# Kernel optimization log

Hardware: AMD Instinct MI355X
Metric: run time of the kernel (lower is better)

Reference implementation:

```python
import jax, jax.numpy as jnp
import numpy as np

_EPS = 1e-5
_NORM_EPS = 1e-6


def setup_inputs() -> dict:
    key = jax.random.key(0)
    k1, k2 = jax.random.split(key)
    B, S, D_IN, D_OUT = 4, 8192, 2048, 2048
    x = jax.random.normal(k1, (B, S, D_IN), dtype=jnp.float32)
    gamma = jnp.ones((D_IN,), dtype=jnp.float32)  # RMSNorm scale
    # kaiming_uniform-like init: bound = sqrt(6/((1+5)*fan_in)) = 1/sqrt(fan_in)
    bound = 1.0 / np.sqrt(D_IN)
    W = jax.random.uniform(k2, (D_OUT, D_IN), dtype=jnp.float32, minval=-bound, maxval=bound)
    return {"x": x, "gamma": gamma, "W": W}


def reference(x, gamma, W):
    # RMSNorm (pre-norm baked into BitLinear)
    rms = jax.lax.rsqrt(jnp.mean(x * x, axis=-1, keepdims=True) + _NORM_EPS)
    xn = x * rms * gamma

    # Per-token absmax int8 activation fake-quant with STE
    a_scale = 127.0 / (jnp.max(jnp.abs(xn), axis=-1, keepdims=True) + _EPS)
    x_q = jnp.clip(jnp.round(xn * a_scale), -128.0, 127.0) / a_scale
    x_ste = xn + jax.lax.stop_gradient(x_q - xn)

    # Per-tensor ternary weight fake-quant (absmean scale) with STE
    w_scale = 1.0 / (jnp.mean(jnp.abs(W)) + _EPS)
    w_q = jnp.clip(jnp.round(W * w_scale), -1.0, 1.0) / w_scale
    w_ste = W + jax.lax.stop_gradient(w_q - W)

    # Linear: [B,S,Din] x [Dout,Din]^T -> [B,S,Dout]
    return jnp.einsum('bsd,od->bso', x_ste, w_ste)
```

## Files before the change

kernel.cpp:

```cpp
#include <hip/hip_runtime.h>
#include <stdint.h>

#define K_DIM 2048
#define N_DIM 2048
#define M_TOK 32768

typedef float v4f __attribute__((ext_vector_type(4)));
typedef int   v4i __attribute__((ext_vector_type(4)));

#define WS_PART   0
#define WS_STAT   8192
#define WS_TSCALE 8448
#define WS_WT     262144
#define WS_QX     4456448

__device__ __forceinline__ void gload_lds16(const void* g, void* l) {
    __builtin_amdgcn_global_load_lds(
        (const __attribute__((address_space(1))) unsigned int*)g,
        (__attribute__((address_space(3))) unsigned int*)l,
        16, 0, 0);
}

__device__ __forceinline__ unsigned int pack4(int a, int b, int c, int d) {
    return (unsigned int)(a & 255) | ((unsigned int)(b & 255) << 8) |
           ((unsigned int)(c & 255) << 16) | ((unsigned int)(d & 255) << 24);
}

__global__ __launch_bounds__(256) void wabs_partial(const float* __restrict__ W,
                                                    double* __restrict__ part) {
    const int t = threadIdx.x, b = blockIdx.x;
    const float* p = W + (size_t)b * 4096;
    double s = 0.0;
#pragma unroll
    for (int i = 0; i < 4; ++i) {
        float4 v = *(const float4*)(p + i * 1024 + t * 4);
        s += (double)fabsf(v.x) + (double)fabsf(v.y) +
             (double)fabsf(v.z) + (double)fabsf(v.w);
    }
    int lane = t & 63, wv = t >> 6;
#pragma unroll
    for (int off = 32; off > 0; off >>= 1) s += __shfl_down(s, off, 64);
    __shared__ double red[4];
    if (lane == 0) red[wv] = s;
    __syncthreads();
    if (t == 0) part[b] = red[0] + red[1] + red[2] + red[3];
}

__global__ __launch_bounds__(256) void wfinal(const double* __restrict__ part,
                                              float* __restrict__ wstat) {
    const int t = threadIdx.x;
    double s = part[t] + part[t + 256] + part[t + 512] + part[t + 768];
    int lane = t & 63, wv = t >> 6;
#pragma unroll
    for (int off = 32; off > 0; off >>= 1) s += __shfl_down(s, off, 64);
    __shared__ double red[4];
    if (lane == 0) red[wv] = s;
    __syncthreads();
    if (t == 0) {
        double mean = (red[0] + red[1] + red[2] + red[3]) * (1.0 / 4194304.0);
        float winv = (float)mean + 1e-5f;
        wstat[0] = winv;
        wstat[1] = 1.0f / winv;
    }
}

__global__ __launch_bounds__(256) void wquant(const float* __restrict__ W,
                                              const float* __restrict__ wstat,
                                              int8_t* __restrict__ wt) {
    const float wsc = wstat[1];
    size_t i = ((size_t)blockIdx.x * 256 + threadIdx.x) * 4;
    float4 v = *(const float4*)(W + i);
    int q0 = (int)rintf(fminf(fmaxf(v.x * wsc, -1.0f), 1.0f));
    int q1 = (int)rintf(fminf(fmaxf(v.y * wsc, -1.0f), 1.0f));
    int q2 = (int)rintf(fminf(fmaxf(v.z * wsc, -1.0f), 1.0f));
    int q3 = (int)rintf(fminf(fmaxf(v.w * wsc, -1.0f), 1.0f));
    *(unsigned int*)(wt + i) = pack4(q0, q1, q2, q3);
}

__global__ __launch_bounds__(256) void rmsnorm_quant(const float* __restrict__ x,
                                                     const float* __restrict__ gamma,
                                                     const float* __restrict__ wstat,
                                                     int8_t* __restrict__ qx,
                                                     float* __restrict__ tscale) {
    const int row = blockIdx.x;
    const int t = threadIdx.x;
    const float* xr = x + (size_t)row * K_DIM;

    float4 v0 = *(const float4*)(xr + t * 4);
    float4 v1 = *(const float4*)(xr + 1024 + t * 4);
    float4 g0 = *(const float4*)(gamma + t * 4);
    float4 g1 = *(const float4*)(gamma + 1024 + t * 4);

    float ss = v0.x * v0.x + v0.y * v0.y + v0.z * v0.z + v0.w * v0.w +
               v1.x * v1.x + v1.y * v1.y + v1.z * v1.z + v1.w * v1.w;

    __shared__ float red[8];
    {
        int lane = t & 63, wv = t >> 6;
#pragma unroll
        for (int off = 32; off > 0; off >>= 1) ss += __shfl_down(ss, off, 64);
        if (lane == 0) red[wv] = ss;
        __syncthreads();
        ss = red[0] + red[1] + red[2] + red[3];
    }
    const float rms = 1.0f / sqrtf(ss * (1.0f / 2048.0f) + 1e-6f);

    float xn[8];
    xn[0] = v0.x * rms * g0.x;  xn[1] = v0.y * rms * g0.y;
    xn[2] = v0.z * rms * g0.z;  xn[3] = v0.w * rms * g0.w;
    xn[4] = v1.x * rms * g1.x;  xn[5] = v1.y * rms * g1.y;
    xn[6] = v1.z * rms * g1.z;  xn[7] = v1.w * rms * g1.w;

    float am = 0.0f;
#pragma unroll
    for (int j = 0; j < 8; ++j) am = fmaxf(am, fabsf(xn[j]));
    {
        int lane = t & 63, wv = t >> 6;
#pragma unroll
        for (int off = 32; off > 0; off >>= 1) am = fmaxf(am, __shfl_down(am, off, 64));
        if (lane == 0) red[4 + wv] = am;
        __syncthreads();
        am = fmaxf(fmaxf(red[4], red[5]), fmaxf(red[6], red[7]));
    }
    const float amp = am + 1e-5f;
    const float ascale = 127.0f / amp;

    int q[8];
#pragma unroll
    for (int j = 0; j < 8; ++j)
        q[j] = (int)rintf(fminf(fmaxf(xn[j] * ascale, -128.0f), 127.0f));

    int8_t* qr = qx + (size_t)row * K_DIM;
    *(unsigned int*)(qr + t * 4)        = pack4(q[0], q[1], q[2], q[3]);
    *(unsigned int*)(qr + 1024 + t * 4) = pack4(q[4], q[5], q[6], q[7]);

    if (t == 0) tscale[row] = amp * wstat[0] * (1.0f / 127.0f);
}


__device__ __forceinline__ v4i ldsfrag(const int8_t* p, int row, int j0) {
    return *(const v4i*)(p + row * 128 + (((j0) ^ (row & 7)) << 4));
}

template <int Q, bool LOADB>
__device__ __forceinline__ void ph_load(const int8_t* pA, const int8_t* pB,
                                        v4i (&af)[2][2], v4i (&bf)[4][2],
                                        int wm, int wn, int l16, int quad) {
    if constexpr (LOADB) {
#pragma unroll
        for (int nt = 0; nt < 4; ++nt)
#pragma unroll
            for (int ks = 0; ks < 2; ++ks)
                bf[nt][ks] = ldsfrag(pB, wn + nt * 16 + l16, ks * 4 + quad);
    }
#pragma unroll
    for (int mt = 0; mt < 2; ++mt)
#pragma unroll
        for (int ks = 0; ks < 2; ++ks)
            af[mt][ks] = ldsfrag(pA, wm + (2 * Q + mt) * 16 + l16, ks * 4 + quad);
}

template <int Q>
__device__ __forceinline__ void ph_mma(v4i (&acc)[8][4], const v4i (&af)[2][2],
                                       const v4i (&bf)[4][2]) {
#pragma unroll
    for (int mt = 0; mt < 2; ++mt)
#pragma unroll
        for (int nt = 0; nt < 4; ++nt)
#pragma unroll
            for (int ks = 0; ks < 2; ++ks)
                acc[2 * Q + mt][nt] = __builtin_amdgcn_mfma_i32_16x16x64_i8(
                    af[mt][ks], bf[nt][ks], acc[2 * Q + mt][nt], 0, 0, 0);
}

#define VMC(n) asm volatile("s_waitcnt vmcnt(" #n ")" ::: "memory")

__global__ __launch_bounds__(512, 2) void gemm_i8(const int8_t* __restrict__ qx,
                                                  const int8_t* __restrict__ wt,
                                                  const float* __restrict__ tscale,
                                                  float* __restrict__ out) {
    __shared__ int8_t ldsA[2][32768];
    __shared__ int8_t ldsB[2][32768];

    const int t = threadIdx.x;
    const int lane = t & 63;
    const int w = t >> 6;
    const int l16 = lane & 15;
    const int quad = lane >> 4;

    const int bid = blockIdx.x;
    const int swz = (bid & 7) * 128 + (bid >> 3);
    const int bn0 = (swz & 7) * 256;
    const int bm0 = (swz >> 3) * 256;

    const int wm = (w >> 2) * 128;
    const int wn = (w & 3) * 64;

    const int srow = t >> 3;
    const int sjx  = ((t & 7) ^ (srow & 7)) << 4;
    const int wbase = w * 1024;
    const size_t baseA = (size_t)bm0 * K_DIM;
    const size_t baseB = (size_t)bn0 * K_DIM;

#define STAGE_A(buf, h, kt) do {                                                   \
        const int8_t* _s = qx + baseA + (size_t)((h) * 128 + srow) * K_DIM +       \
                           (kt) * 128 + sjx;                                       \
        gload_lds16(_s,              &ldsA[buf][(h) * 16384 + wbase]);             \
        gload_lds16(_s + 64 * K_DIM, &ldsA[buf][(h) * 16384 + 8192 + wbase]);      \
    } while (0)
#define STAGE_B(buf, h, kt) do {                                                   \
        const int8_t* _s = wt + baseB + (size_t)((h) * 128 + srow) * K_DIM +       \
                           (kt) * 128 + sjx;                                       \
        gload_lds16(_s,              &ldsB[buf][(h) * 16384 + wbase]);             \
        gload_lds16(_s + 64 * K_DIM, &ldsB[buf][(h) * 16384 + 8192 + wbase]);      \
    } while (0)

    v4i acc[8][4];
    const v4i izero = {0, 0, 0, 0};
#pragma unroll
    for (int i = 0; i < 8; ++i)
#pragma unroll
        for (int j = 0; j < 4; ++j) acc[i][j] = izero;

    v4i bf[4][2];
    const int8_t* pA0 = ldsA[0];
    const int8_t* pA1 = ldsA[1];
    const int8_t* pB0 = ldsB[0];
    const int8_t* pB1 = ldsB[1];

    STAGE_B(0, 0, 0);
    STAGE_B(0, 1, 0);
    STAGE_A(0, 0, 0);
    STAGE_A(0, 1, 0);
    STAGE_B(1, 0, 1);
    STAGE_B(1, 1, 1);
    VMC(4);
    __builtin_amdgcn_s_barrier();

#define DO_PHASE(Q, LOADB, PA, PB, STAGE_STMT, TAIL_STMT)           \
    {                                                               \
        v4i af[2][2];                                               \
        ph_load<Q, LOADB>(PA, PB, af, bf, wm, wn, l16, quad);       \
        STAGE_STMT;                                                 \
        __builtin_amdgcn_s_barrier();                               \
        asm volatile("s_waitcnt lgkmcnt(0)" ::: "memory");          \
        __builtin_amdgcn_sched_barrier(0);                          \
        __builtin_amdgcn_s_setprio(1);                              \
        ph_mma<Q>(acc, af, bf);                                     \
        __builtin_amdgcn_s_setprio(0);                              \
        TAIL_STMT;                                                  \
        __builtin_amdgcn_s_barrier();                               \
    }

#pragma unroll 1
    for (int i = 0; i < 8; ++i) {
        const int kt1 = 2 * i + 1;
        const int kt2 = 2 * i + 2;
        const int kt3 = 2 * i + 3;
        const bool pf = (i < 7);
        DO_PHASE(0, true,  pA0, pB0, STAGE_A(1, 0, kt1), (void)0);
        DO_PHASE(1, false, pA0, pB0, STAGE_A(1, 1, kt1), (void)0);
        DO_PHASE(2, false, pA0, pB0, if (pf) STAGE_B(0, 0, kt2), (void)0);
        DO_PHASE(3, false, pA0, pB0, if (pf) STAGE_B(0, 1, kt2),
                 if (pf) { VMC(4); } else { VMC(0); });
        DO_PHASE(0, true,  pA1, pB1, if (pf) STAGE_A(0, 0, kt2), (void)0);
        DO_PHASE(1, false, pA1, pB1, if (pf) STAGE_A(0, 1, kt2), (void)0);
        DO_PHASE(2, false, pA1, pB1, if (pf) STAGE_B(1, 0, kt3), (void)0);
        DO_PHASE(3, false, pA1, pB1, if (pf) STAGE_B(1, 1, kt3), VMC(4));
    }

#pragma unroll
    for (int mt = 0; mt < 8; ++mt) {
#pragma unroll
        for (int r = 0; r < 4; ++r) {
            const int row = bm0 + wm + mt * 16 + quad * 4 + r;
            const float s = tscale[row];
            float* op = out + (size_t)row * N_DIM + bn0 + wn + l16;
#pragma unroll
            for (int nt = 0; nt < 4; ++nt)
                op[nt * 16] = (float)acc[mt][nt][r] * s;
        }
    }
#undef DO_PHASE
#undef STAGE_A
#undef STAGE_B
}

extern "C" void kernel_launch(void* const* d_in, const int* in_sizes, int n_in,
                              void* d_out, int out_size, void* d_ws, size_t ws_size,
                              hipStream_t stream) {
    const float* x     = (const float*)d_in[0];
    const float* gamma = (const float*)d_in[1];
    const float* W     = (const float*)d_in[2];
    float* out = (float*)d_out;

    char* ws = (char*)d_ws;
    double* wpart  = (double*)(ws + WS_PART);
    float*  wstat  = (float*)(ws + WS_STAT);
    float*  tscale = (float*)(ws + WS_TSCALE);
    int8_t* wt     = (int8_t*)(ws + WS_WT);
    int8_t* qx     = (int8_t*)(ws + WS_QX);

    wabs_partial<<<1024, 256, 0, stream>>>(W, wpart);
    wfinal<<<1, 256, 0, stream>>>(wpart, wstat);
    wquant<<<4096, 256, 0, stream>>>(W, wstat, wt);
    rmsnorm_quant<<<M_TOK, 256, 0, stream>>>(x, gamma, wstat, qx, tscale);

    gemm_i8<<<dim3(1024), dim3(512), 0, stream>>>(qx, wt, tscale, out);
}
```

Baseline: 595.5 us.

## Software-pipeline LDS fragment loads one phase ahead of MFMA in int8 GEMM

Restructures the main loop so that A fragments for the next phase are loaded from LDS into a second register set while the current phase's MFMAs run, using ping-pong af0/af1 buffers and partial lgkmcnt waits. B fragments are reloaded after the last phase of each K-tile, with one barrier per phase removed. This is meant to hide LDS read latency behind matrix-core work. In exchange it raises register pressure under launch_bounds(512,2) and makes the barrier and waitcnt ordering more delicate.

```diff
diff --git a/kernel.cpp b/kernel.cpp
--- a/kernel.cpp
+++ b/kernel.cpp
@@ -142,27 +142,27 @@
     return *(const v4i*)(p + row * 128 + (((j0) ^ (row & 7)) << 4));
 }
 
-template <int Q, bool LOADB>
-__device__ __forceinline__ void ph_load(const int8_t* pA, const int8_t* pB,
-                                        v4i (&af)[2][2], v4i (&bf)[4][2],
-                                        int wm, int wn, int l16, int quad) {
-    if constexpr (LOADB) {
-#pragma unroll
-        for (int nt = 0; nt < 4; ++nt)
-#pragma unroll
-            for (int ks = 0; ks < 2; ++ks)
-                bf[nt][ks] = ldsfrag(pB, wn + nt * 16 + l16, ks * 4 + quad);
-    }
+__device__ __forceinline__ void load_a(v4i (&dst)[2][2], const int8_t* p,
+                                       int q, int wm, int l16, int quad) {
 #pragma unroll
     for (int mt = 0; mt < 2; ++mt)
 #pragma unroll
         for (int ks = 0; ks < 2; ++ks)
-            af[mt][ks] = ldsfrag(pA, wm + (2 * Q + mt) * 16 + l16, ks * 4 + quad);
+            dst[mt][ks] = ldsfrag(p, wm + (2 * q + mt) * 16 + l16, ks * 4 + quad);
+}
+
+__device__ __forceinline__ void load_b(v4i (&dst)[4][2], const int8_t* p,
+                                       int wn, int l16, int quad) {
+#pragma unroll
+    for (int nt = 0; nt < 4; ++nt)
+#pragma unroll
+        for (int ks = 0; ks < 2; ++ks)
+            dst[nt][ks] = ldsfrag(p, wn + nt * 16 + l16, ks * 4 + quad);
 }
 
 template <int Q>
-__device__ __forceinline__ void ph_mma(v4i (&acc)[8][4], const v4i (&af)[2][2],
-                                       const v4i (&bf)[4][2]) {
+__device__ __forceinline__ void mma_q(v4i (&acc)[8][4], const v4i (&af)[2][2],
+                                      const v4i (&bf)[4][2]) {
 #pragma unroll
     for (int mt = 0; mt < 2; ++mt)
 #pragma unroll
@@ -173,7 +173,12 @@
                     af[mt][ks], bf[nt][ks], acc[2 * Q + mt][nt], 0, 0, 0);
 }
 
-#define VMC(n) asm volatile("s_waitcnt vmcnt(" #n ")" ::: "memory")
+#define VMC(n)  asm volatile("s_waitcnt vmcnt(" #n ")" ::: "memory")
+#define LGKM(n) asm volatile("s_waitcnt lgkmcnt(" #n ")" ::: "memory")
+#define SBAR()  __builtin_amdgcn_s_barrier()
+#define SCHEDB() __builtin_amdgcn_sched_barrier(0)
+#define PRIO1() __builtin_amdgcn_s_setprio(1)
+#define PRIO0() __builtin_amdgcn_s_setprio(0)
 
 __global__ __launch_bounds__(512, 2) void gemm_i8(const int8_t* __restrict__ qx,
                                                   const int8_t* __restrict__ wt,
@@ -222,7 +227,7 @@
 #pragma unroll
         for (int j = 0; j < 4; ++j) acc[i][j] = izero;
 
-    v4i bf[4][2];
+    v4i af0[2][2], af1[2][2], bfE[4][2];
     const int8_t* pA0 = ldsA[0];
     const int8_t* pA1 = ldsA[1];
     const int8_t* pB0 = ldsB[0];
@@ -235,22 +240,9 @@
     STAGE_B(1, 0, 1);
     STAGE_B(1, 1, 1);
     VMC(4);
-    __builtin_amdgcn_s_barrier();
-
-#define DO_PHASE(Q, LOADB, PA, PB, STAGE_STMT, TAIL_STMT)           \
-    {                                                               \
-        v4i af[2][2];                                               \
-        ph_load<Q, LOADB>(PA, PB, af, bf, wm, wn, l16, quad);       \
-        STAGE_STMT;                                                 \
-        __builtin_amdgcn_s_barrier();                               \
-        asm volatile("s_waitcnt lgkmcnt(0)" ::: "memory");          \
-        __builtin_amdgcn_sched_barrier(0);                          \
-        __builtin_amdgcn_s_setprio(1);                              \
-        ph_mma<Q>(acc, af, bf);                                     \
-        __builtin_amdgcn_s_setprio(0);                              \
-        TAIL_STMT;                                                  \
-        __builtin_amdgcn_s_barrier();                               \
-    }
+    SBAR();
+    load_b(bfE, pB0, wn, l16, quad);
+    load_a(af0, pA0, 0, wm, l16, quad);
 
 #pragma unroll 1
     for (int i = 0; i < 8; ++i) {
@@ -258,15 +250,62 @@
         const int kt2 = 2 * i + 2;
         const int kt3 = 2 * i + 3;
         const bool pf = (i < 7);
-        DO_PHASE(0, true,  pA0, pB0, STAGE_A(1, 0, kt1), (void)0);
-        DO_PHASE(1, false, pA0, pB0, STAGE_A(1, 1, kt1), (void)0);
-        DO_PHASE(2, false, pA0, pB0, if (pf) STAGE_B(0, 0, kt2), (void)0);
-        DO_PHASE(3, false, pA0, pB0, if (pf) STAGE_B(0, 1, kt2),
-                 if (pf) { VMC(4); } else { VMC(0); });
-        DO_PHASE(0, true,  pA1, pB1, if (pf) STAGE_A(0, 0, kt2), (void)0);
-        DO_PHASE(1, false, pA1, pB1, if (pf) STAGE_A(0, 1, kt2), (void)0);
-        DO_PHASE(2, false, pA1, pB1, if (pf) STAGE_B(1, 0, kt3), (void)0);
-        DO_PHASE(3, false, pA1, pB1, if (pf) STAGE_B(1, 1, kt3), VMC(4));
+
+        STAGE_A(1, 0, kt1);
+        SBAR();
+        load_a(af1, pA0, 1, wm, l16, quad);
+        LGKM(4); SCHEDB();
+        PRIO1(); mma_q<0>(acc, af0, bfE); PRIO0();
+
+        STAGE_A(1, 1, kt1);
+        SBAR();
+        load_a(af0, pA0, 2, wm, l16, quad);
+        LGKM(4); SCHEDB();
+        PRIO1(); mma_q<1>(acc, af1, bfE); PRIO0();
+
+        if (pf) STAGE_B(0, 0, kt2);
+        SBAR();
+        load_a(af1, pA0, 3, wm, l16, quad);
+        LGKM(4); SCHEDB();
+        PRIO1(); mma_q<2>(acc, af0, bfE); PRIO0();
+
+        if (pf) STAGE_B(0, 1, kt2);
+        if (pf) { VMC(4); } else { VMC(0); }
+        SBAR();
+        load_a(af0, pA1, 0, wm, l16, quad);
+        LGKM(4); SCHEDB();
+        PRIO1(); mma_q<3>(acc, af1, bfE); PRIO0();
+        SCHEDB();
+        load_b(bfE, pB1, wn, l16, quad);
+        SBAR();
+
+        if (pf) STAGE_A(0, 0, kt2);
+        SBAR();
+        load_a(af1, pA1, 1, wm, l16, quad);
+        LGKM(4); SCHEDB();
+        PRIO1(); mma_q<0>(acc, af0, bfE); PRIO0();
+
+        if (pf) STAGE_A(0, 1, kt2);
+        SBAR();
+        load_a(af0, pA1, 2, wm, l16, quad);
+        LGKM(4); SCHEDB();
+        PRIO1(); mma_q<1>(acc, af1, bfE); PRIO0();
+
+        if (pf) STAGE_B(1, 0, kt3);
+        SBAR();
+        load_a(af1, pA1, 3, wm, l16, quad);
+        LGKM(4); SCHEDB();
+        PRIO1(); mma_q<2>(acc, af0, bfE); PRIO0();
+
+        if (pf) STAGE_B(1, 1, kt3);
+        if (pf) { VMC(4); } else { VMC(0); }
+        SBAR();
+        if (pf) { load_a(af0, pA0, 0, wm, l16, quad); LGKM(4); } else { LGKM(0); }
+        SCHEDB();
+        PRIO1(); mma_q<3>(acc, af1, bfE); PRIO0();
+        SCHEDB();
+        if (pf) load_b(bfE, pB0, wn, l16, quad);
+        SBAR();
     }
 
 #pragma unroll
@@ -281,7 +320,6 @@
                 op[nt * 16] = (float)acc[mt][nt][r] * s;
         }
     }
-#undef DO_PHASE
 #undef STAGE_A
 #undef STAGE_B
 }
```

After: 603.0 us. About the same (+1.3%).
